# Kernel tuning notes

Hardware: AMD Instinct MI355X
Metric: run time of the kernel (lower is better)

## Reference

```python
import jax, jax.numpy as jnp
import numpy as np

D_MODEL = 4096
N_HEAD = 32
N_KV_HEAD = 8
D_HEAD = D_MODEL // N_HEAD  # 128
B, T = 2, 2048


def setup_inputs() -> dict:
    key = jax.random.key(0)
    ks = jax.random.split(key, 6)
    x = jax.random.normal(ks[0], (B, T, D_MODEL), dtype=jnp.float32)
    # RoPE angles: theta_i = 10000^(-2i/d_head), angle = pos * theta_i
    inv_freq = 1.0 / (10000.0 ** (jnp.arange(0, D_HEAD, 2, dtype=jnp.float32) / D_HEAD))
    angles = jnp.arange(T, dtype=jnp.float32)[:, None] * inv_freq[None, :]  # [T, D_HEAD//2]
    freqs_cos = jnp.cos(angles)
    freqs_sin = jnp.sin(angles)
    s = 0.02
    wq = jax.random.normal(ks[1], (D_MODEL, N_HEAD * D_HEAD), dtype=jnp.float32) * s
    wk = jax.random.normal(ks[2], (D_MODEL, N_KV_HEAD * D_HEAD), dtype=jnp.float32) * s
    wv = jax.random.normal(ks[3], (D_MODEL, N_KV_HEAD * D_HEAD), dtype=jnp.float32) * s
    wo = jax.random.normal(ks[4], (D_MODEL, D_MODEL), dtype=jnp.float32) * s
    return {"x": x, "freqs_cos": freqs_cos, "freqs_sin": freqs_sin,
            "wq": wq, "wk": wk, "wv": wv, "wo": wo}


def _apply_rope(xq, xk, cos, sin):
    # xq: [B,T,Hq,D], xk: [B,T,Hk,D]; cos/sin: [T, D//2]
    def rot(t):
        tr = t.astype(jnp.float32).reshape(*t.shape[:-1], -1, 2)  # [B,T,H,D//2,2]
        xr, xi = tr[..., 0], tr[..., 1]
        c = cos[None, :, None, :]
        s = sin[None, :, None, :]
        out_r = xr * c - xi * s
        out_i = xr * s + xi * c
        return jnp.stack([out_r, out_i], axis=-1).reshape(t.shape).astype(t.dtype)
    return rot(xq), rot(xk)


def reference(x, freqs_cos, freqs_sin, wq, wk, wv, wo):
    Bq, Tq, _ = x.shape
    xq = (x @ wq).reshape(Bq, Tq, N_HEAD, D_HEAD)
    xk = (x @ wk).reshape(Bq, Tq, N_KV_HEAD, D_HEAD)
    xv = (x @ wv).reshape(Bq, Tq, N_KV_HEAD, D_HEAD)
    xq, xk = _apply_rope(xq, xk, freqs_cos, freqs_sin)
    # [B,H,T,D]
    xq = xq.transpose(0, 2, 1, 3)
    xk = xk.transpose(0, 2, 1, 3)
    xv = xv.transpose(0, 2, 1, 3)
    # GQA: repeat kv heads
    rep = N_HEAD // N_KV_HEAD
    xk = jnp.repeat(xk, rep, axis=1)
    xv = jnp.repeat(xv, rep, axis=1)
    scale = 1.0 / np.sqrt(D_HEAD)
    scores = jnp.einsum("bhqd,bhkd->bhqk", xq, xk) * scale
    causal = jnp.tril(jnp.ones((Tq, Tq), dtype=bool))
    scores = jnp.where(causal[None, None], scores, jnp.finfo(scores.dtype).min)
    probs = jax.nn.softmax(scores, axis=-1)
    z = jnp.einsum("bhqk,bhkd->bhqd", probs, xv)
    z = z.transpose(0, 2, 1, 3).reshape(Bq, Tq, D_MODEL)
    return z @ wo
```

## Files before the change

kernel.cpp:

```cpp
#include <hip/hip_runtime.h>

typedef unsigned short u16;
typedef unsigned int u32;
typedef u16 u16x8 __attribute__((ext_vector_type(8)));
typedef __bf16 bf16x8 __attribute__((ext_vector_type(8)));
typedef float f32x4 __attribute__((ext_vector_type(4)));

#define TOKENS 4096
#define DMODEL 4096
#define QKVN 6144
#define NHEAD 32
#define NKV 8
#define DHEAD 128
#define SEQ 2048

#define BARRIER() asm volatile("s_barrier" ::: "memory")
#define LGKM0() asm volatile("s_waitcnt lgkmcnt(0)" ::: "memory")
#define VMCNT(n) asm volatile("s_waitcnt vmcnt(" #n ")" ::: "memory")

__device__ inline u16 f2bf(float f) {
    unsigned int u = __float_as_uint(f);
    u += 0x7fffu + ((u >> 16) & 1u);
    return (u16)(u >> 16);
}
__device__ inline float bf2f(u16 h) {
    return __uint_as_float(((unsigned int)h) << 16);
}
__device__ inline u32 pack2bf(float a, float b) {
    return (u32)f2bf(a) | ((u32)f2bf(b) << 16);
}
__device__ inline f32x4 mfma16(bf16x8 a, bf16x8 b, f32x4 c) {
    return __builtin_amdgcn_mfma_f32_16x16x32_bf16(a, b, c, 0, 0, 0);
}
__device__ __forceinline__ void gload16(const u16* g, u16* l) {
    __builtin_amdgcn_global_load_lds((const __attribute__((address_space(1))) u32*)g,
                                     (__attribute__((address_space(3))) u32*)l, 16, 0, 0);
}

__global__ __launch_bounds__(256) void f2bf_kernel(const float* __restrict__ in,
                                                   u16* __restrict__ out, int n) {
    int i = (blockIdx.x * 256 + threadIdx.x) * 4;
    if (i >= n) return;
    float4 v = *(const float4*)(in + i);
    u16 o0 = f2bf(v.x), o1 = f2bf(v.y), o2 = f2bf(v.z), o3 = f2bf(v.w);
    u16* p = out + i;
    p[0] = o0; p[1] = o1; p[2] = o2; p[3] = o3;
}

__global__ __launch_bounds__(256) void transpose_kernel(const float* __restrict__ in,
                                                        u16* __restrict__ out,
                                                        int K, int N) {
    __shared__ float t[32][33];
    int n0 = blockIdx.x * 32, k0 = blockIdx.y * 32;
    int x = threadIdx.x, y = threadIdx.y;
#pragma unroll
    for (int i = 0; i < 4; i++)
        t[y + 8 * i][x] = in[(size_t)(k0 + y + 8 * i) * N + n0 + x];
    __syncthreads();
#pragma unroll
    for (int i = 0; i < 4; i++)
        out[(size_t)(n0 + y + 8 * i) * K + k0 + x] = f2bf(t[x][y + 8 * i]);
}

__global__ __launch_bounds__(256) void vtrans_kernel(const u16* __restrict__ qkv,
                                                     u16* __restrict__ vt) {
    __shared__ u16 t[32][33];
    int b = blockIdx.z;
    int c0 = blockIdx.x * 32;
    int r0 = blockIdx.y * 32;
    int x = threadIdx.x, y = threadIdx.y;
    const u16* in = qkv + (size_t)(b * SEQ) * QKVN + 5120;
#pragma unroll
    for (int i = 0; i < 4; i++)
        t[y + 8 * i][x] = in[(size_t)(r0 + y + 8 * i) * QKVN + c0 + x];
    __syncthreads();
    u16* out = vt + (size_t)b * 1024 * SEQ;
#pragma unroll
    for (int i = 0; i < 4; i++)
        out[(size_t)(c0 + y + 8 * i) * SEQ + r0 + x] = t[x][y + 8 * i];
}

template <bool OUT_F32>
__global__ __launch_bounds__(512, 2) void gemm256(const u16* __restrict__ A,
                                                  const u16* __restrict__ Bt,
                                                  void* __restrict__ C,
                                                  int M, int N, int K) {
    __shared__ u16 lds[2][2][2][128 * 64];
    const int tid = threadIdx.x, wave = tid >> 6, lane = tid & 63;
    const int quad = lane >> 4, l16 = lane & 15;
    const int wave_m = wave >> 2, wave_n = wave & 3;
    const int m0 = blockIdx.y * 256, n0 = blockIdx.x * 256;
    const int wn = wave_n * 64;
    const int nk = K >> 6;

    const int srow = wave * 16 + (lane >> 3);
    const int scol = ((lane & 7) ^ (lane >> 3)) << 3;
    const u16* ga0 = A + (size_t)(m0 + srow) * K + scol;
    const u16* gb0 = Bt + (size_t)(n0 + srow) * K + scol;

    auto STAGE = [&](int op, int buf, int half, int kt) {
        const u16* src = (op ? gb0 : ga0) + (size_t)(half * 128) * K + (kt << 6);
        u16* dst = &lds[op][buf][half][wave * 1024];
        gload16(src, dst);
        gload16(src + (size_t)8 * K, dst + 512);
    };
    auto FRAG = [&](const u16* base, int lr, int c) -> bf16x8 {
        int idx = (lr * 64 + c) ^ ((lr & 7) << 3);
        return *(const bf16x8*)(base + idx);
    };

    f32x4 acc[8][4] = {};

    STAGE(1, 0, 0, 0); STAGE(1, 0, 1, 0); STAGE(0, 0, 0, 0); STAGE(0, 0, 1, 0);
    STAGE(1, 1, 0, 1); STAGE(1, 1, 1, 1); STAGE(0, 1, 0, 1);
    VMCNT(6);
    BARRIER();

    bf16x8 af[4][2], bfr[4][2];

    auto KTILE = [&](int kt, int cur) {
        const int nxt = cur ^ 1;
        const int k1 = kt + 1 < nk ? kt + 1 : nk - 1;
        const int k2 = kt + 2 < nk ? kt + 2 : nk - 1;
        const u16* aB = &lds[0][cur][wave_m][0];
#pragma unroll
        for (int i = 0; i < 4; i++)
#pragma unroll
            for (int kk = 0; kk < 2; kk++)
                af[i][kk] = FRAG(aB, i * 16 + l16, kk * 32 + quad * 8);
#pragma unroll
        for (int j = 0; j < 4; j++) {
            const int brow = wn + j * 16;
            const u16* bB = &lds[1][cur][brow >> 7][0];
#pragma unroll
            for (int kk = 0; kk < 2; kk++)
                bfr[j][kk] = FRAG(bB, (brow & 127) + l16, kk * 32 + quad * 8);
        }
        STAGE(0, nxt, 1, k1);
        BARRIER();
        __builtin_amdgcn_s_setprio(1);
#pragma unroll
        for (int i = 0; i < 4; i++)
#pragma unroll
            for (int j = 0; j < 2; j++)
#pragma unroll
                for (int kk = 0; kk < 2; kk++)
                    acc[i][j] = mfma16(af[i][kk], bfr[j][kk], acc[i][j]);
        __builtin_amdgcn_s_setprio(0);
        LGKM0();
        BARRIER();
        STAGE(1, cur, 0, k2);
        BARRIER();
        __builtin_amdgcn_s_setprio(1);
#pragma unroll
        for (int i = 0; i < 4; i++)
#pragma unroll
            for (int j = 0; j < 2; j++)
#pragma unroll
                for (int kk = 0; kk < 2; kk++)
                    acc[i][2 + j] = mfma16(af[i][kk], bfr[2 + j][kk], acc[i][2 + j]);
        __builtin_amdgcn_s_setprio(0);
        BARRIER();
#pragma unroll
        for (int i = 0; i < 4; i++)
#pragma unroll
            for (int kk = 0; kk < 2; kk++)
                af[i][kk] = FRAG(aB, 64 + i * 16 + l16, kk * 32 + quad * 8);
        STAGE(1, cur, 1, k2);
        BARRIER();
        __builtin_amdgcn_s_setprio(1);
#pragma unroll
        for (int i = 0; i < 4; i++)
#pragma unroll
            for (int j = 0; j < 2; j++)
#pragma unroll
                for (int kk = 0; kk < 2; kk++)
                    acc[4 + i][j] = mfma16(af[i][kk], bfr[j][kk], acc[4 + i][j]);
        __builtin_amdgcn_s_setprio(0);
        LGKM0();
        BARRIER();
        STAGE(0, cur, 0, k2);
        BARRIER();
        __builtin_amdgcn_s_setprio(1);
#pragma unroll
        for (int i = 0; i < 4; i++)
#pragma unroll
            for (int j = 0; j < 2; j++)
#pragma unroll
                for (int kk = 0; kk < 2; kk++)
                    acc[4 + i][2 + j] = mfma16(af[i][kk], bfr[2 + j][kk], acc[4 + i][2 + j]);
        __builtin_amdgcn_s_setprio(0);
        VMCNT(6);
        BARRIER();
    };

    for (int kt = 0; kt < nk; kt += 2) {
        KTILE(kt, 0);
        KTILE(kt + 1, 1);
    }

    VMCNT(0);

#pragma unroll
    for (int i = 0; i < 8; i++)
#pragma unroll
        for (int j = 0; j < 4; j++) {
            const int row = m0 + wave_m * 128 + i * 16 + quad * 4;
            const int col = n0 + wn + j * 16 + l16;
            if (OUT_F32) {
                float* Cf = (float*)C;
#pragma unroll
                for (int r = 0; r < 4; r++)
                    Cf[(size_t)(row + r) * N + col] = acc[i][j][r];
            } else {
                u16* Cb = (u16*)C;
#pragma unroll
                for (int r = 0; r < 4; r++)
                    Cb[(size_t)(row + r) * N + col] = f2bf(acc[i][j][r]);
            }
        }
}

__global__ __launch_bounds__(256) void rope2_kernel(u16* __restrict__ buf,
                                                    const float* __restrict__ cosb,
                                                    const float* __restrict__ sinb,
                                                    int nheads, int colbase, float scale) {
    int idx = blockIdx.x * 256 + threadIdx.x;
    int p = idx & 63;
    int rest = idx >> 6;
    int h = rest & (nheads - 1);
    int tok = rest / nheads;
    int tseq = tok & (SEQ - 1);
    float c = cosb[tseq * 64 + p], s = sinb[tseq * 64 + p];
    u32* ptr = (u32*)(buf + (size_t)tok * QKVN + colbase + h * DHEAD + 2 * p);
    u32 v = *ptr;
    float xr = bf2f((u16)(v & 0xffff)), xi = bf2f((u16)(v >> 16));
    float orr = (xr * c - xi * s) * scale;
    float oii = (xr * s + xi * c) * scale;
    *ptr = pack2bf(orr, oii);
}

#define LDP 72
#define NINF (-__builtin_inff())

__global__ __launch_bounds__(256, 2) void flash2_kernel(const u16* __restrict__ QKV,
                                                        const u16* __restrict__ Vt,
                                                        u16* __restrict__ Z) {
    __shared__ u16 lK[4][64 * 32];
    __shared__ u16 lV[2][128 * 32];
    __shared__ u16 lP[4][32 * LDP];
    int tid = threadIdx.x, wave = tid >> 6, lane = tid & 63;
    int quad = lane >> 4, l16 = lane & 15;
    int qt = 15 - (int)blockIdx.x;
    int h = blockIdx.y, b = blockIdx.z;
    int kvh = h >> 2;
    int Q0 = qt * 128;
    int qw = Q0 + wave * 32;
    int lrow = lane >> 2, lcol = (lane & 3) * 8;

    bf16x8 qf[2][4];
#pragma unroll
    for (int nt = 0; nt < 2; nt++) {
        const u16* qp = QKV + (size_t)(b * SEQ + qw + nt * 16 + l16) * QKVN + h * DHEAD;
#pragma unroll
        for (int kk = 0; kk < 4; kk++)
            qf[nt][kk] = *(const bf16x8*)(qp + kk * 32 + quad * 8);
    }

    f32x4 o[2][8] = {};
    float mrun[2] = {NINF, NINF};
    float lrun[2] = {0.f, 0.f};

    const u16* gk = QKV + (size_t)(b * SEQ + lrow) * QKVN + DMODEL + kvh * DHEAD + wave * 32 + lcol;
    u16* lk = lK[wave];
    int kf_w = wave >> 1, dh_w = (wave & 1) * 64;
    const u16* gv = Vt + ((size_t)(b * NKV + kvh) * DHEAD + dh_w + lrow) * SEQ + kf_w * 32 + lcol;
    u16* lv = lV[kf_w] + dh_w * 32;

    int nkt = 2 * qt + 2;
    for (int kt = 0; kt < nkt; kt++) {
        int key0 = kt * 64;
        if (kt) __syncthreads();
#pragma unroll
        for (int g = 0; g < 4; g++)
            gload16(gk + (size_t)(key0 + g * 16) * QKVN, lk + g * 512);
#pragma unroll
        for (int g = 0; g < 4; g++)
            gload16(gv + (size_t)(g * 16) * SEQ + key0, lv + g * 512);
        __syncthreads();

        if (key0 <= qw + 31) {
            f32x4 st[4][2] = {};
#pragma unroll
            for (int kk = 0; kk < 4; kk++) {
                bf16x8 kfr[4];
#pragma unroll
                for (int mt = 0; mt < 4; mt++)
                    kfr[mt] = *(const bf16x8*)(lK[kk] + (mt * 16 + l16) * 32 + quad * 8);
#pragma unroll
                for (int mt = 0; mt < 4; mt++)
#pragma unroll
                    for (int nt = 0; nt < 2; nt++)
                        st[mt][nt] = mfma16(kfr[mt], qf[nt][kk], st[mt][nt]);
            }
            if (key0 + 63 > qw) {
#pragma unroll
                for (int mt = 0; mt < 4; mt++)
#pragma unroll
                    for (int nt = 0; nt < 2; nt++)
#pragma unroll
                        for (int r = 0; r < 4; r++)
                            if (key0 + mt * 16 + quad * 4 + r > qw + nt * 16 + l16)
                                st[mt][nt][r] = NINF;
            }
            float alpha[2];
#pragma unroll
            for (int nt = 0; nt < 2; nt++) {
                float vmax = NINF;
#pragma unroll
                for (int mt = 0; mt < 4; mt++)
#pragma unroll
                    for (int r = 0; r < 4; r++) vmax = fmaxf(vmax, st[mt][nt][r]);
                vmax = fmaxf(vmax, __shfl_xor(vmax, 16));
                vmax = fmaxf(vmax, __shfl_xor(vmax, 32));
                float mnew = fmaxf(mrun[nt], vmax);
                alpha[nt] = __expf(mrun[nt] - mnew);
                mrun[nt] = mnew;
                float rsum = 0.f;
#pragma unroll
                for (int mt = 0; mt < 4; mt++)
#pragma unroll
                    for (int r = 0; r < 4; r++) {
                        float p = __expf(st[mt][nt][r] - mnew);
                        st[mt][nt][r] = p;
                        rsum += p;
                    }
                rsum += __shfl_xor(rsum, 16);
                rsum += __shfl_xor(rsum, 32);
                lrun[nt] = lrun[nt] * alpha[nt] + rsum;
#pragma unroll
                for (int mt = 0; mt < 4; mt++) {
                    u32 p01 = pack2bf(st[mt][nt][0], st[mt][nt][1]);
                    u32 p23 = pack2bf(st[mt][nt][2], st[mt][nt][3]);
                    uint2 pk; pk.x = p01; pk.y = p23;
                    *(uint2*)(lP[wave] + (nt * 16 + l16) * LDP + mt * 16 + quad * 4) = pk;
                }
            }
#pragma unroll
            for (int mtq = 0; mtq < 2; mtq++)
#pragma unroll
                for (int r = 0; r < 4; r++) {
                    float av = __shfl(alpha[mtq], quad * 4 + r);
#pragma unroll
                    for (int ntd = 0; ntd < 8; ntd++) o[mtq][ntd][r] *= av;
                }
#pragma unroll
            for (int kfi = 0; kfi < 2; kfi++) {
                bf16x8 pf0 = *(const bf16x8*)(lP[wave] + l16 * LDP + kfi * 32 + quad * 8);
                bf16x8 pf1 = *(const bf16x8*)(lP[wave] + (16 + l16) * LDP + kfi * 32 + quad * 8);
#pragma unroll
                for (int ntd = 0; ntd < 8; ntd++) {
                    bf16x8 vfr = *(const bf16x8*)(lV[kfi] + (ntd * 16 + l16) * 32 + quad * 8);
                    o[0][ntd] = mfma16(pf0, vfr, o[0][ntd]);
                    o[1][ntd] = mfma16(pf1, vfr, o[1][ntd]);
                }
            }
        }
    }
#pragma unroll
    for (int mtq = 0; mtq < 2; mtq++) {
        float linv[4];
#pragma unroll
        for (int r = 0; r < 4; r++) linv[r] = 1.0f / __shfl(lrun[mtq], quad * 4 + r);
#pragma unroll
        for (int ntd = 0; ntd < 8; ntd++)
#pragma unroll
            for (int r = 0; r < 4; r++) {
                int q = qw + mtq * 16 + quad * 4 + r;
                Z[(size_t)(b * SEQ + q) * DMODEL + h * DHEAD + ntd * 16 + l16] =
                    f2bf(o[mtq][ntd][r] * linv[r]);
            }
    }
}

extern "C" void kernel_launch(void* const* d_in, const int* in_sizes, int n_in,
                              void* d_out, int out_size, void* d_ws, size_t ws_size,
                              hipStream_t stream) {
    const float* x    = (const float*)d_in[0];
    const float* fcos = (const float*)d_in[1];
    const float* fsin = (const float*)d_in[2];
    const float* wq   = (const float*)d_in[3];
    const float* wk   = (const float*)d_in[4];
    const float* wv   = (const float*)d_in[5];
    const float* wo   = (const float*)d_in[6];
    float* out = (float*)d_out;
    char* ws = (char*)d_ws;

    const size_t MiB = 1024ull * 1024ull;
    u16* xb    = (u16*)(ws);
    u16* zb    = xb;
    u16* wqkvt = (u16*)(ws + 32 * MiB);
    u16* wot   = (u16*)(ws + 80 * MiB);
    u16* qkv   = (u16*)(ws + 112 * MiB);
    u16* vtb   = (u16*)(ws + 160 * MiB);

    f2bf_kernel<<<16384, 256, 0, stream>>>(x, xb, TOKENS * DMODEL);
    dim3 tb(32, 8);
    transpose_kernel<<<dim3(128, 128), tb, 0, stream>>>(wq, wqkvt, 4096, 4096);
    transpose_kernel<<<dim3(32, 128), tb, 0, stream>>>(wk, wqkvt + (size_t)4096 * 4096, 4096, 1024);
    transpose_kernel<<<dim3(32, 128), tb, 0, stream>>>(wv, wqkvt + (size_t)5120 * 4096, 4096, 1024);
    transpose_kernel<<<dim3(128, 128), tb, 0, stream>>>(wo, wot, 4096, 4096);

    gemm256<false><<<dim3(24, 16), 512, 0, stream>>>(xb, wqkvt, qkv, 4096, QKVN, 4096);

    rope2_kernel<<<32768, 256, 0, stream>>>(qkv, fcos, fsin, NHEAD, 0, 0.08838834764831845f);
    rope2_kernel<<<8192, 256, 0, stream>>>(qkv, fcos, fsin, NKV, DMODEL, 1.0f);

    vtrans_kernel<<<dim3(32, 64, 2), tb, 0, stream>>>(qkv, vtb);

    flash2_kernel<<<dim3(16, 32, 2), 256, 0, stream>>>(qkv, vtb, zb);

    gemm256<true><<<dim3(16, 16), 512, 0, stream>>>(zb, wot, out, 4096, 4096, 4096);
}
```

Measured before the change: 768.0 us.

## Double-buffer K/V tiles in flash attention to overlap loads with compute

Splits the K and V shared-memory tiles into two buffers and issues the global-to-LDS loads for the next key tile before computing on the current one. A partial vmcnt wait replaces the two full barriers around each load, so tile fetches can overlap the MFMA work. The P scratch buffer is also re-laid out as two 32-wide chunks without padding. Shared memory use roughly doubles, which may cut occupancy below two blocks per CU, and the unpadded P layout may add LDS bank conflicts.

```diff
diff --git a/kernel.cpp b/kernel.cpp
--- a/kernel.cpp
+++ b/kernel.cpp
@@ -240,15 +240,14 @@
     *ptr = pack2bf(orr, oii);
 }
 
-#define LDP 72
 #define NINF (-__builtin_inff())
 
 __global__ __launch_bounds__(256, 2) void flash2_kernel(const u16* __restrict__ QKV,
                                                         const u16* __restrict__ Vt,
                                                         u16* __restrict__ Z) {
-    __shared__ u16 lK[4][64 * 32];
-    __shared__ u16 lV[2][128 * 32];
-    __shared__ u16 lP[4][32 * LDP];
+    __shared__ u16 lK[2][4][64 * 32];
+    __shared__ u16 lV[2][2][128 * 32];
+    __shared__ u16 lP[4][2][32 * 32];
     int tid = threadIdx.x, wave = tid >> 6, lane = tid & 63;
     int quad = lane >> 4, l16 = lane & 15;
     int qt = 15 - (int)blockIdx.x;
@@ -272,23 +271,32 @@
     float lrun[2] = {0.f, 0.f};
 
     const u16* gk = QKV + (size_t)(b * SEQ + lrow) * QKVN + DMODEL + kvh * DHEAD + wave * 32 + lcol;
-    u16* lk = lK[wave];
     int kf_w = wave >> 1, dh_w = (wave & 1) * 64;
     const u16* gv = Vt + ((size_t)(b * NKV + kvh) * DHEAD + dh_w + lrow) * SEQ + kf_w * 32 + lcol;
-    u16* lv = lV[kf_w] + dh_w * 32;
-
-    int nkt = 2 * qt + 2;
-    for (int kt = 0; kt < nkt; kt++) {
+
+    auto STAGEKV = [&](int kt, int buf) {
         int key0 = kt * 64;
-        if (kt) __syncthreads();
+        u16* lk = lK[buf][wave];
+        u16* lv = lV[buf][kf_w] + dh_w * 32;
 #pragma unroll
         for (int g = 0; g < 4; g++)
             gload16(gk + (size_t)(key0 + g * 16) * QKVN, lk + g * 512);
 #pragma unroll
         for (int g = 0; g < 4; g++)
             gload16(gv + (size_t)(g * 16) * SEQ + key0, lv + g * 512);
-        __syncthreads();
-
+    };
+
+    int nkt = 2 * qt + 2;
+    STAGEKV(0, 0);
+
+    for (int kt = 0; kt < nkt; kt++) {
+        int cur = kt & 1;
+        int ks = (kt + 1 < nkt) ? kt + 1 : nkt - 1;
+        STAGEKV(ks, cur ^ 1);
+        VMCNT(8);
+        BARRIER();
+
+        int key0 = kt * 64;
         if (key0 <= qw + 31) {
             f32x4 st[4][2] = {};
 #pragma unroll
@@ -296,7 +304,7 @@
                 bf16x8 kfr[4];
 #pragma unroll
                 for (int mt = 0; mt < 4; mt++)
-                    kfr[mt] = *(const bf16x8*)(lK[kk] + (mt * 16 + l16) * 32 + quad * 8);
+                    kfr[mt] = *(const bf16x8*)(lK[cur][kk] + (mt * 16 + l16) * 32 + quad * 8);
 #pragma unroll
                 for (int mt = 0; mt < 4; mt++)
 #pragma unroll
@@ -343,7 +351,7 @@
                     u32 p01 = pack2bf(st[mt][nt][0], st[mt][nt][1]);
                     u32 p23 = pack2bf(st[mt][nt][2], st[mt][nt][3]);
                     uint2 pk; pk.x = p01; pk.y = p23;
-                    *(uint2*)(lP[wave] + (nt * 16 + l16) * LDP + mt * 16 + quad * 4) = pk;
+                    *(uint2*)(lP[wave][mt >> 1] + (nt * 16 + l16) * 32 + (mt & 1) * 16 + quad * 4) = pk;
                 }
             }
 #pragma unroll
@@ -356,17 +364,21 @@
                 }
 #pragma unroll
             for (int kfi = 0; kfi < 2; kfi++) {
-                bf16x8 pf0 = *(const bf16x8*)(lP[wave] + l16 * LDP + kfi * 32 + quad * 8);
-                bf16x8 pf1 = *(const bf16x8*)(lP[wave] + (16 + l16) * LDP + kfi * 32 + quad * 8);
+                bf16x8 pf0 = *(const bf16x8*)(lP[wave][kfi] + l16 * 32 + quad * 8);
+                bf16x8 pf1 = *(const bf16x8*)(lP[wave][kfi] + (16 + l16) * 32 + quad * 8);
 #pragma unroll
                 for (int ntd = 0; ntd < 8; ntd++) {
-                    bf16x8 vfr = *(const bf16x8*)(lV[kfi] + (ntd * 16 + l16) * 32 + quad * 8);
+                    bf16x8 vfr = *(const bf16x8*)(lV[cur][kfi] + (ntd * 16 + l16) * 32 + quad * 8);
                     o[0][ntd] = mfma16(pf0, vfr, o[0][ntd]);
                     o[1][ntd] = mfma16(pf1, vfr, o[1][ntd]);
                 }
             }
         }
+        LGKM0();
+        BARRIER();
     }
+    VMCNT(0);
+
 #pragma unroll
     for (int mtq = 0; mtq < 2; mtq++) {
         float linv[4];
```

Result: slower. 785.4 us (+2.3%).
